# Performance work log

Measured on AMD Instinct MI355X. Metric: run time of the kernel, lower is better.

The kernel has to match this reference:

```python
import jax, jax.numpy as jnp
import numpy as np

N = 100000
E = 1000000
F_IN = 64
HID = 128
NCLS = 32
G = 1024
EPS = 1e-5


def setup_inputs() -> dict:
    key = jax.random.key(0)
    ks = jax.random.split(key, 6)
    x = jax.random.normal(ks[0], (N, F_IN), dtype=jnp.float32)
    edge_index = jax.random.randint(ks[1], (2, E), 0, N, dtype=jnp.int64)
    batch = jnp.sort(jax.random.randint(ks[2], (N,), 0, G, dtype=jnp.int64))
    # parameters (init per _init_weights: uniform(-0.01,0.01) linears, BN w=0.1 b=0)
    W_gcn = jax.random.uniform(ks[3], (F_IN, HID), minval=-0.01, maxval=0.01, dtype=jnp.float32)
    b_gcn = jnp.zeros((HID,), jnp.float32)
    bn1_w = jnp.full((HID,), 0.1, jnp.float32)
    bn1_b = jnp.zeros((HID,), jnp.float32)
    W_out = jax.random.uniform(ks[4], (HID, NCLS), minval=-0.01, maxval=0.01, dtype=jnp.float32)
    b_out = jnp.zeros((NCLS,), jnp.float32)
    bn2_w = jnp.full((NCLS,), 0.1, jnp.float32)
    bn2_b = jnp.zeros((NCLS,), jnp.float32)
    return {"x": x, "edge_index": edge_index, "batch": batch,
            "W_gcn": W_gcn, "b_gcn": b_gcn, "bn1_w": bn1_w, "bn1_b": bn1_b,
            "W_out": W_out, "b_out": b_out, "bn2_w": bn2_w, "bn2_b": bn2_b}


def _batchnorm(h, w, b):
    # training-mode BN: biased batch statistics over dim 0
    mu = jnp.mean(h, axis=0)
    var = jnp.var(h, axis=0)
    return (h - mu) * jax.lax.rsqrt(var + EPS) * w + b


def reference(x, edge_index, batch, W_gcn, b_gcn, bn1_w, bn1_b, W_out, b_out, bn2_w, bn2_b):
    # --- GCNConv: add self loops, symmetric norm, transform, aggregate ---
    loop = jnp.arange(N, dtype=edge_index.dtype)
    src = jnp.concatenate([edge_index[0], loop])  # [E+N]
    dst = jnp.concatenate([edge_index[1], loop])
    deg = jax.ops.segment_sum(jnp.ones_like(dst, dtype=x.dtype), dst, num_segments=N)
    dinv = jax.lax.rsqrt(deg)  # deg >= 1 thanks to self loops
    coef = dinv[src] * dinv[dst]  # [E+N]
    h = x @ W_gcn  # [N, HID] transform before gather (as PyG)
    msg = h[src] * coef[:, None]  # [E+N, HID] gathered messages
    h = jax.ops.segment_sum(msg, dst, num_segments=N) + b_gcn
    # --- BN + ReLU (dropout is identity in eval) ---
    h = jax.nn.relu(_batchnorm(h, bn1_w, bn1_b))
    # --- global_mean_pool over graphs ---
    sums = jax.ops.segment_sum(h, batch, num_segments=G)  # [G, HID]
    cnt = jax.ops.segment_sum(jnp.ones((N,), h.dtype), batch, num_segments=G)
    pooled = sums / jnp.maximum(cnt, 1.0)[:, None]
    # --- head: Linear + BN ---
    out = pooled @ W_out + b_out
    return _batchnorm(out, bn2_w, bn2_b)
```

## Files before the change

### kernel.cpp

```cpp
#include <hip/hip_runtime.h>
#include <hip/hip_fp16.h>

constexpr int N    = 100000;
constexpr int E    = 1000000;
constexpr int FIN  = 64;
constexpr int HID  = 128;
constexpr int NCLS = 32;
constexpr int G    = 1024;
constexpr float EPS = 1e-5f;

constexpr int NTILE = (N + 127) / 128;

constexpr int NBUCK = 98;
constexpr int NPB   = 1024;
constexpr int EPB   = 4096;
constexpr int CAP   = 12288;
constexpr int BIN_GRID = (E + EPB - 1) / EPB;

typedef _Float16 half2v __attribute__((ext_vector_type(2)));

__device__ inline float fdot2f(__half2 a, __half2 b, float c) {
#if __has_builtin(__builtin_amdgcn_fdot2)
  return __builtin_amdgcn_fdot2(*(half2v*)&a, *(half2v*)&b, c, false);
#else
  float2 fa = __half22float2(a), fb = __half22float2(b);
  return c + fa.x * fb.x + fa.y * fb.y;
#endif
}

__global__ __launch_bounds__(256) void k_bin(const int* __restrict__ src,
                                             const int* __restrict__ dst,
                                             int* __restrict__ bucketCursor,
                                             uint2* __restrict__ bucketBuf) {
  __shared__ int bcnt[NBUCK];
  __shared__ int bdelta[NBUCK];
  __shared__ int lcur[NBUCK];
  __shared__ int part[128];
  __shared__ uint2 staged[EPB];
  int tid = threadIdx.x;
  int e0 = blockIdx.x * EPB;
  int cnt = E - e0 < EPB ? E - e0 : EPB;
  for (int i = tid; i < NBUCK; i += 256) bcnt[i] = 0;
  __syncthreads();
  for (int i = tid; i < cnt; i += 256) {
    int d = dst[e0 + i];
    atomicAdd(&bcnt[d >> 10], 1);
  }
  __syncthreads();
  if (tid < 128) part[tid] = (tid < NBUCK) ? bcnt[tid] : 0;
  __syncthreads();
  for (int off = 1; off < 128; off <<= 1) {
    int t = 0;
    if (tid < 128 && tid >= off) t = part[tid - off];
    __syncthreads();
    if (tid < 128) part[tid] += t;
    __syncthreads();
  }
  if (tid < NBUCK) {
    int excl = part[tid] - bcnt[tid];
    int base = bcnt[tid] ? atomicAdd(&bucketCursor[tid], bcnt[tid]) : 0;
    bdelta[tid] = base - excl;
    lcur[tid]   = excl;
  }
  __syncthreads();
  for (int i = tid; i < cnt; i += 256) {
    int s = src[e0 + i], d = dst[e0 + i];
    int pos = atomicAdd(&lcur[d >> 10], 1);
    staged[pos] = make_uint2((unsigned)s, (unsigned)d);
  }
  __syncthreads();
  for (int i = tid; i < cnt; i += 256) {
    uint2 p = staged[i];
    int b = (int)(p.y >> 10);
    bucketBuf[(long long)b * CAP + bdelta[b] + i] = p;
  }
}

__global__ __launch_bounds__(1024) void k_build(const int* __restrict__ bucketLen,
                                                const uint2* __restrict__ bucketBuf,
                                                int* __restrict__ offsets,
                                                float* __restrict__ dinv,
                                                int* __restrict__ srclist) {
  __shared__ int cnt[NPB];
  __shared__ int part[1024];
  __shared__ int sh_bbase;
  int b = blockIdx.x, tid = threadIdx.x;
  int n0 = b << 10;
  int nn = (N - n0 < NPB) ? (N - n0) : NPB;
  int len = bucketLen[b];
  cnt[tid] = 0;
  if (tid < 128) part[tid] = (tid < NBUCK) ? bucketLen[tid] : 0;
  __syncthreads();
  for (int off = 1; off < 128; off <<= 1) {
    int t = 0;
    if (tid < 128 && tid >= off) t = part[tid - off];
    __syncthreads();
    if (tid < 128) part[tid] += t;
    __syncthreads();
  }
  if (tid == b) sh_bbase = part[b] - len;
  __syncthreads();
  const uint2* buf = bucketBuf + (long long)b * CAP;
  for (int i = tid; i < len; i += 1024)
    atomicAdd(&cnt[(int)buf[i].y - n0], 1);
  __syncthreads();
  int v = cnt[tid];
  part[tid] = v;
  __syncthreads();
  for (int off = 1; off < 1024; off <<= 1) {
    int t = (tid >= off) ? part[tid - off] : 0;
    __syncthreads();
    part[tid] += t;
    __syncthreads();
  }
  int base = sh_bbase;
  int o = base + part[tid] - v;
  __syncthreads();
  cnt[tid] = o;
  if (tid < nn) {
    offsets[n0 + tid] = o;
    dinv[n0 + tid] = rsqrtf((float)v + 1.0f);
  }
  if (b == NBUCK - 1 && tid == 1023) offsets[N] = base + part[1023];
  __syncthreads();
  for (int i = tid; i < len; i += 1024) {
    uint2 p = buf[i];
    int pos = atomicAdd(&cnt[(int)p.y - n0], 1);
    srclist[pos] = (int)p.x;
  }
}

__global__ void k_scale(const float4* __restrict__ x4, const float* __restrict__ dinv,
                        float2* __restrict__ y2) {
  int i = blockIdx.x * blockDim.x + threadIdx.x;
  if (i >= N * 16) return;
  int node = i >> 4;
  float c = dinv[node];
  float4 v = x4[i];
  union { float2 f; __half2 h[2]; } u;
  u.h[0] = __float22half2_rn(make_float2(v.x * c, v.y * c));
  u.h[1] = __float22half2_rn(make_float2(v.z * c, v.w * c));
  y2[i] = u.f;
}

__global__ void k_wprep(const float* __restrict__ W, __half2* __restrict__ w2g,
                        int* __restrict__ bucketCursor, float* __restrict__ sums) {
  int idx = blockIdx.x * blockDim.x + threadIdx.x;
  if (blockIdx.x == 0 && threadIdx.x < 128) bucketCursor[threadIdx.x] = 0;
  if (blockIdx.x == 1 && threadIdx.x < 64) {
    float* p = sums + threadIdx.x;
    p[0] = 0.f; p[64] = 0.f; p[128] = 0.f; p[192] = 0.f; p[256] = 0.f;
  }
  if (idx >= 32 * 128) return;
  int kp = idx >> 7, col = idx & 127;
  w2g[idx] = __floats2half2_rn(W[(2 * kp) * 128 + col], W[(2 * kp + 1) * 128 + col]);
}

__global__ __launch_bounds__(256) void k_gather(const int* __restrict__ offsets,
                                                const int* __restrict__ srclist,
                                                const float* __restrict__ dinv,
                                                const float2* __restrict__ y2,
                                                float2* __restrict__ aggh) {
  int node = blockIdx.x * 16 + (threadIdx.x >> 4);
  int lane = threadIdx.x & 15;
  if (node >= N) return;
  int start = offsets[node], end = offsets[node + 1];
  float cd = dinv[node];

  union { float2 f; __half2 h[2]; } u;
  float4 a0, a1, a2, a3;
  u.f = y2[node * 16 + lane];
  {
    float2 f01 = __half22float2(u.h[0]);
    float2 f23 = __half22float2(u.h[1]);
    a0 = make_float4(f01.x, f01.y, f23.x, f23.y);
  }
  a1 = make_float4(0.f, 0.f, 0.f, 0.f);
  a2 = a1; a3 = a1;

  int i = start;
  for (; i + 3 < end; i += 4) {
    int s0 = srclist[i], s1 = srclist[i + 1], s2 = srclist[i + 2], s3 = srclist[i + 3];
    union { float2 f; __half2 h[2]; } u0, u1, u2, u3;
    u0.f = y2[(long long)s0 * 16 + lane];
    u1.f = y2[(long long)s1 * 16 + lane];
    u2.f = y2[(long long)s2 * 16 + lane];
    u3.f = y2[(long long)s3 * 16 + lane];
    float2 p, q;
    p = __half22float2(u0.h[0]); q = __half22float2(u0.h[1]);
    a0.x += p.x; a0.y += p.y; a0.z += q.x; a0.w += q.y;
    p = __half22float2(u1.h[0]); q = __half22float2(u1.h[1]);
    a1.x += p.x; a1.y += p.y; a1.z += q.x; a1.w += q.y;
    p = __half22float2(u2.h[0]); q = __half22float2(u2.h[1]);
    a2.x += p.x; a2.y += p.y; a2.z += q.x; a2.w += q.y;
    p = __half22float2(u3.h[0]); q = __half22float2(u3.h[1]);
    a3.x += p.x; a3.y += p.y; a3.z += q.x; a3.w += q.y;
  }
  for (; i < end; ++i) {
    int s = srclist[i];
    u.f = y2[(long long)s * 16 + lane];
    float2 p = __half22float2(u.h[0]);
    float2 q = __half22float2(u.h[1]);
    a0.x += p.x; a0.y += p.y; a0.z += q.x; a0.w += q.y;
  }
  float4 acc;
  acc.x = ((a0.x + a1.x) + (a2.x + a3.x)) * cd;
  acc.y = ((a0.y + a1.y) + (a2.y + a3.y)) * cd;
  acc.z = ((a0.z + a1.z) + (a2.z + a3.z)) * cd;
  acc.w = ((a0.w + a1.w) + (a2.w + a3.w)) * cd;
  union { float2 f; __half2 h[2]; } o;
  o.h[0] = __floats2half2_rn(acc.x, acc.y);
  o.h[1] = __floats2half2_rn(acc.z, acc.w);
  aggh[node * 16 + lane] = o.f;
}

__global__ __launch_bounds__(256) void k_gemm2h(const __half2* __restrict__ aggh2,
                                                const __half2* __restrict__ w2g,
                                                const float* __restrict__ b,
                                                __half2* __restrict__ h2,
                                                float* __restrict__ sums) {
  __shared__ __half2 Wl[32 * 128];
  __shared__ __half2 rowT[32 * 128];
  int tid  = threadIdx.x;
  int row0 = blockIdx.x * 128;
  {
    const float4* srcv = (const float4*)w2g;
    float4* dstv = (float4*)Wl;
    for (int i = tid; i < 1024; i += 256) dstv[i] = srcv[i];
  }
  {
    int half = tid >> 7;
    int r = tid & 127;
    int grow = row0 + r;
#pragma unroll
    for (int c = 0; c < 4; ++c) {
      int kp0 = half * 16 + c * 4;
      float4 v = make_float4(0.f, 0.f, 0.f, 0.f);
      if (grow < N) v = *(const float4*)&aggh2[(long long)grow * 32 + kp0];
      __half2* pv = (__half2*)&v;
      rowT[(kp0 + 0) * 128 + r] = pv[0];
      rowT[(kp0 + 1) * 128 + r] = pv[1];
      rowT[(kp0 + 2) * 128 + r] = pv[2];
      rowT[(kp0 + 3) * 128 + r] = pv[3];
    }
  }
  __syncthreads();

  int rt = tid >> 4, ct = tid & 15;
  float acc[8][8];
#pragma unroll
  for (int m = 0; m < 8; ++m)
#pragma unroll
    for (int j = 0; j < 8; ++j) acc[m][j] = 0.f;

#pragma unroll 2
  for (int kp = 0; kp < 32; ++kp) {
    float4 wv0 = *(const float4*)&Wl[kp * 128 + ct * 8];
    float4 wv1 = *(const float4*)&Wl[kp * 128 + ct * 8 + 4];
    float4 rv0 = *(const float4*)&rowT[kp * 128 + rt * 8];
    float4 rv1 = *(const float4*)&rowT[kp * 128 + rt * 8 + 4];
    __half2 wv[8], rv[8];
    *(float4*)&wv[0] = wv0; *(float4*)&wv[4] = wv1;
    *(float4*)&rv[0] = rv0; *(float4*)&rv[4] = rv1;
#pragma unroll
    for (int m = 0; m < 8; ++m)
#pragma unroll
      for (int j = 0; j < 8; ++j) acc[m][j] = fdot2f(rv[m], wv[j], acc[m][j]);
  }

  int cbase = ct * 8;
  float4 b0 = *(const float4*)&b[cbase];
  float4 b1 = *(const float4*)&b[cbase + 4];
  float bias[8] = {b0.x, b0.y, b0.z, b0.w, b1.x, b1.y, b1.z, b1.w};
  float s[8], s2[8];
#pragma unroll
  for (int j = 0; j < 8; ++j) { s[j] = 0.f; s2[j] = 0.f; }
#pragma unroll
  for (int m = 0; m < 8; ++m) {
    int grow = row0 + rt * 8 + m;
    if (grow < N) {
      float hv[8];
#pragma unroll
      for (int j = 0; j < 8; ++j) {
        hv[j] = acc[m][j] + bias[j];
        s[j] += hv[j];
        s2[j] += hv[j] * hv[j];
      }
      union { float4 f; __half2 h[4]; } o;
      o.h[0] = __floats2half2_rn(hv[0], hv[1]);
      o.h[1] = __floats2half2_rn(hv[2], hv[3]);
      o.h[2] = __floats2half2_rn(hv[4], hv[5]);
      o.h[3] = __floats2half2_rn(hv[6], hv[7]);
      *(float4*)&h2[(long long)grow * 64 + ct * 4] = o.f;
    }
  }
  __syncthreads();
  float* red = (float*)Wl;
#pragma unroll
  for (int j = 0; j < 8; ++j) {
    red[rt * 256 + cbase + j]       = s[j];
    red[rt * 256 + 128 + cbase + j] = s2[j];
  }
  __syncthreads();
  float tot = 0.f;
#pragma unroll 4
  for (int r = 0; r < 16; ++r) tot += red[r * 256 + tid];
  atomicAdd(&sums[tid], tot);
}

__global__ __launch_bounds__(128) void k_bn1_final(const float* __restrict__ sums,
                                                   const float* __restrict__ w,
                                                   const float* __restrict__ bb,
                                                   float* __restrict__ ss) {
  int tid = threadIdx.x;
  float mu  = sums[tid] * (1.0f / N);
  float var = sums[tid + 128] * (1.0f / N) - mu * mu;
  float rs  = rsqrtf(var + EPS);
  float sc  = rs * w[tid];
  ss[tid]       = sc;
  ss[tid + 128] = bb[tid] - mu * sc;
}

__global__ __launch_bounds__(256) void k_pool(const __half2* __restrict__ h2,
                                              const float* __restrict__ ss,
                                              const int* __restrict__ batch,
                                              float* __restrict__ pooled) {
  int g = blockIdx.x;
  int lo = 0, hi = N;
  while (lo < hi) { int m = (lo + hi) >> 1; if (batch[m] < g) lo = m + 1; else hi = m; }
  int lo2 = lo, hi2 = N;
  while (lo2 < hi2) { int m = (lo2 + hi2) >> 1; if (batch[m] < g + 1) lo2 = m + 1; else hi2 = m; }
  int start = lo, end = lo2;
  int tid = threadIdx.x;
  int cp = tid & 63, rp = tid >> 6;
  float sc0 = ss[2 * cp], sc1 = ss[2 * cp + 1];
  float sh0 = ss[2 * cp + 128], sh1 = ss[2 * cp + 129];
  float s0 = 0.f, s1 = 0.f;
  for (int r = start + rp; r < end; r += 4) {
    float2 f = __half22float2(h2[(long long)r * 64 + cp]);
    s0 += fmaxf(f.x * sc0 + sh0, 0.f);
    s1 += fmaxf(f.y * sc1 + sh1, 0.f);
  }
  __shared__ float red0[256], red1[256];
  red0[tid] = s0; red1[tid] = s1;
  __syncthreads();
  if (tid < 64) {
#pragma unroll
    for (int q = 1; q < 4; ++q) { s0 += red0[tid + q * 64]; s1 += red1[tid + q * 64]; }
    float cnt = fmaxf((float)(end - start), 1.0f);
    float2 o = make_float2(s0 / cnt, s1 / cnt);
    *(float2*)&pooled[g * 128 + 2 * tid] = o;
  }
}

__global__ __launch_bounds__(256) void k_head(const float* __restrict__ pooled,
                                              const float* __restrict__ W,
                                              const float* __restrict__ b,
                                              float* __restrict__ outpre,
                                              float* __restrict__ sums2) {
  int idx = blockIdx.x * 256 + threadIdx.x;
  int g = idx >> 5, c = idx & 31;
  float acc = b[c];
  const float* pr = pooled + g * 128;
#pragma unroll
  for (int k = 0; k < 128; ++k) acc += pr[k] * W[k * 32 + c];
  outpre[idx] = acc;
  __shared__ float red[256], red2[256];
  int tid = threadIdx.x;
  red[tid] = acc; red2[tid] = acc * acc;
  __syncthreads();
  for (int off = 128; off >= 32; off >>= 1) {
    if (tid < off) { red[tid] += red[tid + off]; red2[tid] += red2[tid + off]; }
    __syncthreads();
  }
  if (tid < 32) {
    atomicAdd(&sums2[tid], red[tid]);
    atomicAdd(&sums2[tid + 32], red2[tid]);
  }
}

__global__ void k_bn2f(const float* __restrict__ sums2, const float* __restrict__ w,
                       const float* __restrict__ b, float* __restrict__ ss2) {
  int c = threadIdx.x;
  float mu  = sums2[c] * (1.0f / G);
  float var = sums2[c + 32] * (1.0f / G) - mu * mu;
  float rs  = rsqrtf(var + EPS);
  float sc  = rs * w[c];
  ss2[c]      = sc;
  ss2[c + 32] = b[c] - mu * sc;
}

__global__ void k_bn2apply(const float* __restrict__ outpre, const float* __restrict__ ss2,
                           float* __restrict__ out) {
  int idx = blockIdx.x * 256 + threadIdx.x;
  int c = idx & 31;
  out[idx] = outpre[idx] * ss2[c] + ss2[c + 32];
}

extern "C" void kernel_launch(void* const* d_in, const int* in_sizes, int n_in,
                              void* d_out, int out_size, void* d_ws, size_t ws_size,
                              hipStream_t stream) {
  const float* x   = (const float*)d_in[0];
  const int* ei    = (const int*)d_in[1];
  const int* batch = (const int*)d_in[2];
  const float* Wg  = (const float*)d_in[3];
  const float* bg  = (const float*)d_in[4];
  const float* w1  = (const float*)d_in[5];
  const float* b1  = (const float*)d_in[6];
  const float* Wo  = (const float*)d_in[7];
  const float* bo  = (const float*)d_in[8];
  const float* w2  = (const float*)d_in[9];
  const float* b2  = (const float*)d_in[10];

  float* ws     = (float*)d_ws;
  float* dinv   = ws;
  float* aggh_f = ws + 100352;
  float* h2_f   = aggh_f + 1600512;
  float* ss     = h2_f + 6400000;
  float* sums   = ss + 256;
  float* sums2  = sums + 256;
  float* ss2    = sums2 + 64;
  float* pooled = ss2 + 64;
  float* outpre = pooled + G * 128;
  int* offsets  = (int*)(outpre + G * 32);
  int* srclist  = offsets + 100416;
  int* bucketCursor = srclist + E;
  __half2* w2g  = (__half2*)(bucketCursor + 128);
  uint2* bucketBuf = (uint2*)h2_f;
  float2* y2       = (float2*)(h2_f + 3100000);

  const int* src = ei;
  const int* dst = ei + E;

  k_wprep<<<16, 256, 0, stream>>>(Wg, w2g, bucketCursor, sums);
  k_bin<<<BIN_GRID, 256, 0, stream>>>(src, dst, bucketCursor, bucketBuf);
  k_build<<<NBUCK, 1024, 0, stream>>>(bucketCursor, bucketBuf, offsets, dinv, srclist);
  k_scale<<<(N * 16 + 255) / 256, 256, 0, stream>>>((const float4*)x, dinv, y2);
  k_gather<<<(N + 15) / 16, 256, 0, stream>>>(offsets, srclist, dinv, y2, (float2*)aggh_f);
  k_gemm2h<<<NTILE, 256, 0, stream>>>((const __half2*)aggh_f, w2g, bg,
                                      (__half2*)h2_f, sums);
  k_bn1_final<<<1, 128, 0, stream>>>(sums, w1, b1, ss);
  k_pool<<<G, 256, 0, stream>>>((const __half2*)h2_f, ss, batch, pooled);
  k_head<<<128, 256, 0, stream>>>(pooled, Wo, bo, outpre, sums2);
  k_bn2f<<<1, 32, 0, stream>>>(sums2, w2, b2, ss2);
  k_bn2apply<<<128, 256, 0, stream>>>(outpre, ss2, (float*)d_out);
}
```

Measured before the change: 217.9 us.

## Fuse neighbor gather into GEMM kernel and pack binned edges into 32-bit words

Merges the CSR gather kernel into the half-precision GEMM kernel, so aggregated rows go straight into shared memory instead of a global intermediate buffer. The fused kernel uses 512 threads per 128-row tile with a 4x8 accumulator per thread. Separately, edge binning now packs the local destination (10 bits) and source (17 bits) into one 32-bit word, which halves bucket buffer traffic, and doubles edges per binning block. The scatter recovers each edge's bucket with a binary search over the prefix array. Risks include lower gather parallelism per block and extra search work in the scatter.

```diff
diff --git a/kernel.cpp b/kernel.cpp
--- a/kernel.cpp
+++ b/kernel.cpp
@@ -13,7 +13,7 @@
 
 constexpr int NBUCK = 98;
 constexpr int NPB   = 1024;
-constexpr int EPB   = 4096;
+constexpr int EPB   = 8192;
 constexpr int CAP   = 12288;
 constexpr int BIN_GRID = (E + EPB - 1) / EPB;
 
@@ -31,33 +31,32 @@
 __global__ __launch_bounds__(256) void k_bin(const int* __restrict__ src,
                                              const int* __restrict__ dst,
                                              int* __restrict__ bucketCursor,
-                                             uint2* __restrict__ bucketBuf) {
+                                             unsigned* __restrict__ bucketBuf) {
   __shared__ int bcnt[NBUCK];
+  __shared__ int incl[128];
   __shared__ int bdelta[NBUCK];
   __shared__ int lcur[NBUCK];
-  __shared__ int part[128];
-  __shared__ uint2 staged[EPB];
+  __shared__ unsigned staged[EPB];
   int tid = threadIdx.x;
   int e0 = blockIdx.x * EPB;
   int cnt = E - e0 < EPB ? E - e0 : EPB;
   for (int i = tid; i < NBUCK; i += 256) bcnt[i] = 0;
   __syncthreads();
   for (int i = tid; i < cnt; i += 256) {
-    int d = dst[e0 + i];
-    atomicAdd(&bcnt[d >> 10], 1);
-  }
-  __syncthreads();
-  if (tid < 128) part[tid] = (tid < NBUCK) ? bcnt[tid] : 0;
+    atomicAdd(&bcnt[dst[e0 + i] >> 10], 1);
+  }
+  __syncthreads();
+  if (tid < 128) incl[tid] = (tid < NBUCK) ? bcnt[tid] : 0;
   __syncthreads();
   for (int off = 1; off < 128; off <<= 1) {
     int t = 0;
-    if (tid < 128 && tid >= off) t = part[tid - off];
-    __syncthreads();
-    if (tid < 128) part[tid] += t;
+    if (tid < 128 && tid >= off) t = incl[tid - off];
+    __syncthreads();
+    if (tid < 128) incl[tid] += t;
     __syncthreads();
   }
   if (tid < NBUCK) {
-    int excl = part[tid] - bcnt[tid];
+    int excl = incl[tid] - bcnt[tid];
     int base = bcnt[tid] ? atomicAdd(&bucketCursor[tid], bcnt[tid]) : 0;
     bdelta[tid] = base - excl;
     lcur[tid]   = excl;
@@ -66,18 +65,19 @@
   for (int i = tid; i < cnt; i += 256) {
     int s = src[e0 + i], d = dst[e0 + i];
     int pos = atomicAdd(&lcur[d >> 10], 1);
-    staged[pos] = make_uint2((unsigned)s, (unsigned)d);
+    staged[pos] = ((unsigned)(d & 1023) << 17) | (unsigned)s;
   }
   __syncthreads();
   for (int i = tid; i < cnt; i += 256) {
-    uint2 p = staged[i];
-    int b = (int)(p.y >> 10);
-    bucketBuf[(long long)b * CAP + bdelta[b] + i] = p;
+    unsigned p = staged[i];
+    int lo = 0, hi = NBUCK - 1;
+    while (lo < hi) { int m = (lo + hi) >> 1; if (incl[m] > i) hi = m; else lo = m + 1; }
+    bucketBuf[(long long)lo * CAP + bdelta[lo] + i] = p;
   }
 }
 
 __global__ __launch_bounds__(1024) void k_build(const int* __restrict__ bucketLen,
-                                                const uint2* __restrict__ bucketBuf,
+                                                const unsigned* __restrict__ bucketBuf,
                                                 int* __restrict__ offsets,
                                                 float* __restrict__ dinv,
                                                 int* __restrict__ srclist) {
@@ -100,9 +100,9 @@
   }
   if (tid == b) sh_bbase = part[b] - len;
   __syncthreads();
-  const uint2* buf = bucketBuf + (long long)b * CAP;
+  const unsigned* buf = bucketBuf + (long long)b * CAP;
   for (int i = tid; i < len; i += 1024)
-    atomicAdd(&cnt[(int)buf[i].y - n0], 1);
+    atomicAdd(&cnt[buf[i] >> 17], 1);
   __syncthreads();
   int v = cnt[tid];
   part[tid] = v;
@@ -113,20 +113,19 @@
     part[tid] += t;
     __syncthreads();
   }
-  int base = sh_bbase;
-  int o = base + part[tid] - v;
+  int o = sh_bbase + part[tid] - v;
   __syncthreads();
   cnt[tid] = o;
   if (tid < nn) {
     offsets[n0 + tid] = o;
     dinv[n0 + tid] = rsqrtf((float)v + 1.0f);
   }
-  if (b == NBUCK - 1 && tid == 1023) offsets[N] = base + part[1023];
+  if (b == NBUCK - 1 && tid == 1023) offsets[N] = sh_bbase + part[1023];
   __syncthreads();
   for (int i = tid; i < len; i += 1024) {
-    uint2 p = buf[i];
-    int pos = atomicAdd(&cnt[(int)p.y - n0], 1);
-    srclist[pos] = (int)p.x;
+    unsigned p = buf[i];
+    int pos = atomicAdd(&cnt[p >> 17], 1);
+    srclist[pos] = (int)(p & 0x1FFFFu);
   }
 }
 
@@ -156,114 +155,95 @@
   w2g[idx] = __floats2half2_rn(W[(2 * kp) * 128 + col], W[(2 * kp + 1) * 128 + col]);
 }
 
-__global__ __launch_bounds__(256) void k_gather(const int* __restrict__ offsets,
-                                                const int* __restrict__ srclist,
-                                                const float* __restrict__ dinv,
-                                                const float2* __restrict__ y2,
-                                                float2* __restrict__ aggh) {
-  int node = blockIdx.x * 16 + (threadIdx.x >> 4);
-  int lane = threadIdx.x & 15;
-  if (node >= N) return;
-  int start = offsets[node], end = offsets[node + 1];
-  float cd = dinv[node];
-
-  union { float2 f; __half2 h[2]; } u;
-  float4 a0, a1, a2, a3;
-  u.f = y2[node * 16 + lane];
-  {
-    float2 f01 = __half22float2(u.h[0]);
-    float2 f23 = __half22float2(u.h[1]);
-    a0 = make_float4(f01.x, f01.y, f23.x, f23.y);
-  }
-  a1 = make_float4(0.f, 0.f, 0.f, 0.f);
-  a2 = a1; a3 = a1;
-
-  int i = start;
-  for (; i + 3 < end; i += 4) {
-    int s0 = srclist[i], s1 = srclist[i + 1], s2 = srclist[i + 2], s3 = srclist[i + 3];
-    union { float2 f; __half2 h[2]; } u0, u1, u2, u3;
-    u0.f = y2[(long long)s0 * 16 + lane];
-    u1.f = y2[(long long)s1 * 16 + lane];
-    u2.f = y2[(long long)s2 * 16 + lane];
-    u3.f = y2[(long long)s3 * 16 + lane];
-    float2 p, q;
-    p = __half22float2(u0.h[0]); q = __half22float2(u0.h[1]);
-    a0.x += p.x; a0.y += p.y; a0.z += q.x; a0.w += q.y;
-    p = __half22float2(u1.h[0]); q = __half22float2(u1.h[1]);
-    a1.x += p.x; a1.y += p.y; a1.z += q.x; a1.w += q.y;
-    p = __half22float2(u2.h[0]); q = __half22float2(u2.h[1]);
-    a2.x += p.x; a2.y += p.y; a2.z += q.x; a2.w += q.y;
-    p = __half22float2(u3.h[0]); q = __half22float2(u3.h[1]);
-    a3.x += p.x; a3.y += p.y; a3.z += q.x; a3.w += q.y;
-  }
-  for (; i < end; ++i) {
-    int s = srclist[i];
-    u.f = y2[(long long)s * 16 + lane];
-    float2 p = __half22float2(u.h[0]);
-    float2 q = __half22float2(u.h[1]);
-    a0.x += p.x; a0.y += p.y; a0.z += q.x; a0.w += q.y;
-  }
-  float4 acc;
-  acc.x = ((a0.x + a1.x) + (a2.x + a3.x)) * cd;
-  acc.y = ((a0.y + a1.y) + (a2.y + a3.y)) * cd;
-  acc.z = ((a0.z + a1.z) + (a2.z + a3.z)) * cd;
-  acc.w = ((a0.w + a1.w) + (a2.w + a3.w)) * cd;
-  union { float2 f; __half2 h[2]; } o;
-  o.h[0] = __floats2half2_rn(acc.x, acc.y);
-  o.h[1] = __floats2half2_rn(acc.z, acc.w);
-  aggh[node * 16 + lane] = o.f;
-}
-
-__global__ __launch_bounds__(256) void k_gemm2h(const __half2* __restrict__ aggh2,
-                                                const __half2* __restrict__ w2g,
-                                                const float* __restrict__ b,
-                                                __half2* __restrict__ h2,
-                                                float* __restrict__ sums) {
-  __shared__ __half2 Wl[32 * 128];
-  __shared__ __half2 rowT[32 * 128];
+__global__ __launch_bounds__(512) void k_gg(const int* __restrict__ offsets,
+                                            const int* __restrict__ srclist,
+                                            const float* __restrict__ dinv,
+                                            const float2* __restrict__ y2,
+                                            const __half2* __restrict__ w2g,
+                                            const float* __restrict__ b,
+                                            __half2* __restrict__ h2,
+                                            float* __restrict__ sums) {
+  __shared__ __align__(16) char smem[32 * 1024];
+  __half2* Wl   = (__half2*)smem;
+  __half2* rowT = (__half2*)smem + 4096;
   int tid  = threadIdx.x;
   int row0 = blockIdx.x * 128;
   {
-    const float4* srcv = (const float4*)w2g;
-    float4* dstv = (float4*)Wl;
-    for (int i = tid; i < 1024; i += 256) dstv[i] = srcv[i];
+    const float4* s4 = (const float4*)w2g;
+    float4* d4 = (float4*)Wl;
+    for (int i = tid; i < 1024; i += 512) d4[i] = s4[i];
   }
   {
-    int half = tid >> 7;
-    int r = tid & 127;
-    int grow = row0 + r;
-#pragma unroll
-    for (int c = 0; c < 4; ++c) {
-      int kp0 = half * 16 + c * 4;
-      float4 v = make_float4(0.f, 0.f, 0.f, 0.f);
-      if (grow < N) v = *(const float4*)&aggh2[(long long)grow * 32 + kp0];
-      __half2* pv = (__half2*)&v;
-      rowT[(kp0 + 0) * 128 + r] = pv[0];
-      rowT[(kp0 + 1) * 128 + r] = pv[1];
-      rowT[(kp0 + 2) * 128 + r] = pv[2];
-      rowT[(kp0 + 3) * 128 + r] = pv[3];
+    int grp = tid >> 4, lane = tid & 15;
+#pragma unroll
+    for (int it = 0; it < 4; ++it) {
+      int r = it * 32 + grp;
+      int node = row0 + r;
+      float4 a0 = make_float4(0.f, 0.f, 0.f, 0.f), a1 = a0, a2 = a0, a3 = a0;
+      if (node < N) {
+        int start = offsets[node], end = offsets[node + 1];
+        float cd = dinv[node];
+        union { float2 f; __half2 h[2]; } u;
+        u.f = y2[(long long)node * 16 + lane];
+        {
+          float2 p = __half22float2(u.h[0]), q = __half22float2(u.h[1]);
+          a0 = make_float4(p.x, p.y, q.x, q.y);
+        }
+        int i = start;
+        for (; i + 3 < end; i += 4) {
+          int s0 = srclist[i], s1 = srclist[i + 1], s2 = srclist[i + 2], s3 = srclist[i + 3];
+          union { float2 f; __half2 h[2]; } u0, u1, u2, u3;
+          u0.f = y2[(long long)s0 * 16 + lane];
+          u1.f = y2[(long long)s1 * 16 + lane];
+          u2.f = y2[(long long)s2 * 16 + lane];
+          u3.f = y2[(long long)s3 * 16 + lane];
+          float2 p, q;
+          p = __half22float2(u0.h[0]); q = __half22float2(u0.h[1]);
+          a0.x += p.x; a0.y += p.y; a0.z += q.x; a0.w += q.y;
+          p = __half22float2(u1.h[0]); q = __half22float2(u1.h[1]);
+          a1.x += p.x; a1.y += p.y; a1.z += q.x; a1.w += q.y;
+          p = __half22float2(u2.h[0]); q = __half22float2(u2.h[1]);
+          a2.x += p.x; a2.y += p.y; a2.z += q.x; a2.w += q.y;
+          p = __half22float2(u3.h[0]); q = __half22float2(u3.h[1]);
+          a3.x += p.x; a3.y += p.y; a3.z += q.x; a3.w += q.y;
+        }
+        for (; i < end; ++i) {
+          int s = srclist[i];
+          u.f = y2[(long long)s * 16 + lane];
+          float2 p = __half22float2(u.h[0]);
+          float2 q = __half22float2(u.h[1]);
+          a0.x += p.x; a0.y += p.y; a0.z += q.x; a0.w += q.y;
+        }
+        float sx = ((a0.x + a1.x) + (a2.x + a3.x)) * cd;
+        float sy = ((a0.y + a1.y) + (a2.y + a3.y)) * cd;
+        float sz = ((a0.z + a1.z) + (a2.z + a3.z)) * cd;
+        float sw = ((a0.w + a1.w) + (a2.w + a3.w)) * cd;
+        rowT[(2 * lane) * 128 + r]     = __floats2half2_rn(sx, sy);
+        rowT[(2 * lane + 1) * 128 + r] = __floats2half2_rn(sz, sw);
+      } else {
+        rowT[(2 * lane) * 128 + r]     = __floats2half2_rn(0.f, 0.f);
+        rowT[(2 * lane + 1) * 128 + r] = __floats2half2_rn(0.f, 0.f);
+      }
     }
   }
   __syncthreads();
-
   int rt = tid >> 4, ct = tid & 15;
-  float acc[8][8];
-#pragma unroll
-  for (int m = 0; m < 8; ++m)
+  float acc[4][8];
+#pragma unroll
+  for (int m = 0; m < 4; ++m)
 #pragma unroll
     for (int j = 0; j < 8; ++j) acc[m][j] = 0.f;
 
-#pragma unroll 2
+#pragma unroll 4
   for (int kp = 0; kp < 32; ++kp) {
+    float4 rv4 = *(const float4*)&rowT[kp * 128 + rt * 4];
     float4 wv0 = *(const float4*)&Wl[kp * 128 + ct * 8];
     float4 wv1 = *(const float4*)&Wl[kp * 128 + ct * 8 + 4];
-    float4 rv0 = *(const float4*)&rowT[kp * 128 + rt * 8];
-    float4 rv1 = *(const float4*)&rowT[kp * 128 + rt * 8 + 4];
-    __half2 wv[8], rv[8];
+    __half2 rv[4], wv[8];
+    *(float4*)&rv[0] = rv4;
     *(float4*)&wv[0] = wv0; *(float4*)&wv[4] = wv1;
-    *(float4*)&rv[0] = rv0; *(float4*)&rv[4] = rv1;
-#pragma unroll
-    for (int m = 0; m < 8; ++m)
+#pragma unroll
+    for (int m = 0; m < 4; ++m)
 #pragma unroll
       for (int j = 0; j < 8; ++j) acc[m][j] = fdot2f(rv[m], wv[j], acc[m][j]);
   }
@@ -276,8 +256,8 @@
 #pragma unroll
   for (int j = 0; j < 8; ++j) { s[j] = 0.f; s2[j] = 0.f; }
 #pragma unroll
-  for (int m = 0; m < 8; ++m) {
-    int grow = row0 + rt * 8 + m;
+  for (int m = 0; m < 4; ++m) {
+    int grow = row0 + rt * 4 + m;
     if (grow < N) {
       float hv[8];
 #pragma unroll
@@ -295,17 +275,19 @@
     }
   }
   __syncthreads();
-  float* red = (float*)Wl;
+  float* red = (float*)smem;
 #pragma unroll
   for (int j = 0; j < 8; ++j) {
     red[rt * 256 + cbase + j]       = s[j];
     red[rt * 256 + 128 + cbase + j] = s2[j];
   }
   __syncthreads();
-  float tot = 0.f;
+  if (tid < 256) {
+    float tot = 0.f;
 #pragma unroll 4
-  for (int r = 0; r < 16; ++r) tot += red[r * 256 + tid];
-  atomicAdd(&sums[tid], tot);
+    for (int r = 0; r < 32; ++r) tot += red[r * 256 + tid];
+    atomicAdd(&sums[tid], tot);
+  }
 }
 
 __global__ __launch_bounds__(128) void k_bn1_final(const float* __restrict__ sums,
@@ -414,9 +396,9 @@
 
   float* ws     = (float*)d_ws;
   float* dinv   = ws;
-  float* aggh_f = ws + 100352;
-  float* h2_f   = aggh_f + 1600512;
-  float* ss     = h2_f + 6400000;
+  float* y2f    = dinv + 100352;
+  float* h2f    = y2f + 3200000;
+  float* ss     = h2f + 6400000;
   float* sums   = ss + 256;
   float* sums2  = sums + 256;
   float* ss2    = sums2 + 64;
@@ -426,8 +408,7 @@
   int* srclist  = offsets + 100416;
   int* bucketCursor = srclist + E;
   __half2* w2g  = (__half2*)(bucketCursor + 128);
-  uint2* bucketBuf = (uint2*)h2_f;
-  float2* y2       = (float2*)(h2_f + 3100000);
+  unsigned* bucketBuf = (unsigned*)((float*)w2g + 4096);
 
   const int* src = ei;
   const int* dst = ei + E;
@@ -435,12 +416,11 @@
   k_wprep<<<16, 256, 0, stream>>>(Wg, w2g, bucketCursor, sums);
   k_bin<<<BIN_GRID, 256, 0, stream>>>(src, dst, bucketCursor, bucketBuf);
   k_build<<<NBUCK, 1024, 0, stream>>>(bucketCursor, bucketBuf, offsets, dinv, srclist);
-  k_scale<<<(N * 16 + 255) / 256, 256, 0, stream>>>((const float4*)x, dinv, y2);
-  k_gather<<<(N + 15) / 16, 256, 0, stream>>>(offsets, srclist, dinv, y2, (float2*)aggh_f);
-  k_gemm2h<<<NTILE, 256, 0, stream>>>((const __half2*)aggh_f, w2g, bg,
-                                      (__half2*)h2_f, sums);
+  k_scale<<<(N * 16 + 255) / 256, 256, 0, stream>>>((const float4*)x, dinv, (float2*)y2f);
+  k_gg<<<NTILE, 512, 0, stream>>>(offsets, srclist, dinv, (const float2*)y2f,
+                                  w2g, bg, (__half2*)h2f, sums);
   k_bn1_final<<<1, 128, 0, stream>>>(sums, w1, b1, ss);
-  k_pool<<<G, 256, 0, stream>>>((const __half2*)h2_f, ss, batch, pooled);
+  k_pool<<<G, 256, 0, stream>>>((const __half2*)h2f, ss, batch, pooled);
   k_head<<<128, 256, 0, stream>>>(pooled, Wo, bo, outpre, sums2);
   k_bn2f<<<1, 32, 0, stream>>>(sums2, w2, b2, ss2);
   k_bn2apply<<<128, 256, 0, stream>>>(outpre, ss2, (float*)d_out);
```

Result: slower. 244.0 us (+12.0%).
